# Kernel optimization log

Measured on AMD Instinct MI355X. Metric: run time of the kernel, lower is better.

## Reference

```python
import jax, jax.numpy as jnp
import numpy as np

N = 2_000_000
G = 10_000
NGQ = 5
_X_KS, _W_KS = np.polynomial.hermite.hermgauss(NGQ)


def setup_inputs() -> dict:
    key = jax.random.key(0)
    k1, k2, k3 = jax.random.split(key, 3)
    y_true = jax.random.bernoulli(k1, 0.5, (N, 1)).astype(jnp.float32)
    y_pred = jax.random.normal(k2, (N, 1), dtype=jnp.float32)
    Z_idx = jax.random.randint(k3, (N,), 0, G, dtype=jnp.int32)
    sig2b = jnp.array(1.0, dtype=jnp.float32)  # self.sig2bs[0]
    return {"y_true": y_true, "y_pred": y_pred, "sig2b": sig2b,
            "Z_idx": Z_idx, "n_groups": G}


def reference(y_true, y_pred, sig2b, Z_idx, n_groups):
    y = y_true[:, 0]  # [N]
    f = y_pred[:, 0]  # [N]
    x_ks = jnp.asarray(_X_KS, dtype=f.dtype)  # [K]
    w_ks = jnp.asarray(_W_KS, dtype=f.dtype)  # [K]
    # c_k = sqrt(2) * sqrt(sig2b) * x_k
    c = jnp.sqrt(jnp.asarray(2.0, f.dtype)) * jnp.sqrt(sig2b) * x_ks  # [K]
    # Per-group sufficient statistics (replaces the per-unique-group Python loop)
    yf_g = jax.ops.segment_sum(y * f, Z_idx, num_segments=n_groups)      # [G]
    ysum_g = jax.ops.segment_sum(y, Z_idx, num_segments=n_groups)        # [G]
    # log(1 + exp(f_i + c_k)) summed within each group -> [G, K]
    lg = jax.ops.segment_sum(jnp.log1p(jnp.exp(f[:, None] + c[None, :])),
                             Z_idx, num_segments=n_groups)
    expnt = yf_g[:, None] + ysum_g[:, None] * c[None, :] - lg            # [G, K]
    inv_sqrt_pi = 1.0 / np.sqrt(np.pi)
    k_sum = jnp.sum(jnp.exp(expnt) * (w_ks * inv_sqrt_pi)[None, :], axis=1)  # [G]
    total = -jnp.sum(jnp.log(k_sum))
    return total.reshape(1, 1)
```

## Files before the change

kernel.cpp:

```cpp
#include <hip/hip_runtime.h>
#include <math.h>


#define NG 10000
#define COPIES 256
#define ATHREADS 1024
#define ESCALE 16.0f
#define LN2ESC 11.090354888959125f
#define FMASK12 0xFFFull
#define LN2F 0.6931471805599453f
#define INVLN2F 1.4426950408889634f

__device__ __forceinline__ unsigned int spq(float x) {
    float e2 = __builtin_amdgcn_exp2f(-fabsf(x) * INVLN2F);
    float lg = __builtin_amdgcn_logf(1.0f + e2);
    return (unsigned int)(fmaxf(x, 0.0f) * ESCALE + lg * LN2ESC + 0.5f);
}

__device__ __forceinline__ unsigned long long compute_pack(float yi, float fi,
                                                           const float* ck) {
    float sy = 1.0f - 2.0f * yi;
    unsigned long long p = 0ull;
#pragma unroll
    for (int k = 0; k < 5; ++k) {
        unsigned int u = spq(sy * (fi + ck[k]));
        p |= (unsigned long long)u << (12 * k);
    }
    return p;
}


__global__ __launch_bounds__(ATHREADS) void copnll_accum_lds(
        const float* __restrict__ y, const float* __restrict__ f,
        const float* __restrict__ sig2b, const int* __restrict__ z,
        unsigned long long* __restrict__ partials,
        float* __restrict__ out, int n) {
    __shared__ __align__(16) unsigned long long lds[NG];

    const float s = sqrtf(2.0f) * sqrtf(sig2b[0]);
    const float xks[5] = {-2.0201828704560856f, -0.9585724646138185f, 0.0f,
                          0.9585724646138185f, 2.0201828704560856f};
    float ck[5];
#pragma unroll
    for (int k = 0; k < 5; ++k) ck[k] = s * xks[k];

    const float4* y4 = (const float4*)y;
    const float4* f4 = (const float4*)f;
    const int4*   z4 = (const int4*)z;
    int n4 = n >> 2;
    int t = blockIdx.x * ATHREADS + threadIdx.x;
    int total = gridDim.x * ATHREADS;
    int i0 = t, i1 = t + total;
    bool h0 = i0 < n4, h1 = i1 < n4;

    float4 ya, fa, yb, fb;
    int4 za, zb;
    if (h0) { ya = y4[i0]; fa = f4[i0]; za = z4[i0]; }
    if (h1) { yb = y4[i1]; fb = f4[i1]; zb = z4[i1]; }

    for (int j = threadIdx.x; j < NG; j += ATHREADS) lds[j] = 0ull;
    if (blockIdx.x == 0 && threadIdx.x == 0) out[0] = 0.0f;
    __syncthreads();

    if (h0) {
        atomicAdd(&lds[za.x], compute_pack(ya.x, fa.x, ck));
        atomicAdd(&lds[za.y], compute_pack(ya.y, fa.y, ck));
        atomicAdd(&lds[za.z], compute_pack(ya.z, fa.z, ck));
        atomicAdd(&lds[za.w], compute_pack(ya.w, fa.w, ck));
    }
    if (h1) {
        atomicAdd(&lds[zb.x], compute_pack(yb.x, fb.x, ck));
        atomicAdd(&lds[zb.y], compute_pack(yb.y, fb.y, ck));
        atomicAdd(&lds[zb.z], compute_pack(yb.z, fb.z, ck));
        atomicAdd(&lds[zb.w], compute_pack(yb.w, fb.w, ck));
    }
    for (int i = t + 2 * total; i < n4; i += total) {
        float4 yv = y4[i];
        float4 fv = f4[i];
        int4   zv = z4[i];
        atomicAdd(&lds[zv.x], compute_pack(yv.x, fv.x, ck));
        atomicAdd(&lds[zv.y], compute_pack(yv.y, fv.y, ck));
        atomicAdd(&lds[zv.z], compute_pack(yv.z, fv.z, ck));
        atomicAdd(&lds[zv.w], compute_pack(yv.w, fv.w, ck));
    }
    if (blockIdx.x == 0 && (int)threadIdx.x < (n & 3)) {
        int i = (n4 << 2) + threadIdx.x;
        atomicAdd(&lds[z[i]], compute_pack(y[i], f[i], ck));
    }
    __syncthreads();

    ulonglong2* dst = (ulonglong2*)(partials + (size_t)blockIdx.x * NG);
    const ulonglong2* src = (const ulonglong2*)lds;
    for (int j = threadIdx.x; j < NG / 2; j += ATHREADS) dst[j] = src[j];
}

#define GPB 64
#define SUBS 4
__global__ __launch_bounds__(256) void copnll_merge(
        const unsigned long long* __restrict__ partials,
        float* __restrict__ out) {
    const float wn[5] = {0.011257411327720683f, 0.22207592200561263f,
                         0.53333333333333333f, 0.22207592200561263f,
                         0.011257411327720683f};
    __shared__ unsigned int comb[SUBS][GPB][5];

    int gl  = threadIdx.x & 63;
    int sub = threadIdx.x >> 6;
    int g = blockIdx.x * GPB + gl;
    unsigned int fs0 = 0, fs1 = 0, fs2 = 0, fs3 = 0, fs4 = 0;
    if (g < NG) {
        const unsigned long long* base =
            partials + (size_t)sub * (COPIES / SUBS) * NG + g;
#pragma unroll 8
        for (int j = 0; j < COPIES / SUBS; ++j) {
            unsigned long long q = base[(size_t)j * NG];
            fs0 += (unsigned int)(q & FMASK12);
            fs1 += (unsigned int)((q >> 12) & FMASK12);
            fs2 += (unsigned int)((q >> 24) & FMASK12);
            fs3 += (unsigned int)((q >> 36) & FMASK12);
            fs4 += (unsigned int)((q >> 48) & FMASK12);
        }
    }
    comb[sub][gl][0] = fs0;
    comb[sub][gl][1] = fs1;
    comb[sub][gl][2] = fs2;
    comb[sub][gl][3] = fs3;
    comb[sub][gl][4] = fs4;
    __syncthreads();

    if (threadIdx.x < 64) {
        float local = 0.0f;
        if (g < NG) {
            unsigned int t0 = 0, t1 = 0, t2 = 0, t3 = 0, t4 = 0;
#pragma unroll
            for (int s2 = 0; s2 < SUBS; ++s2) {
                t0 += comb[s2][gl][0];
                t1 += comb[s2][gl][1];
                t2 += comb[s2][gl][2];
                t3 += comb[s2][gl][3];
                t4 += comb[s2][gl][4];
            }
            float ek[5];
            ek[0] = -(float)t0 * (1.0f / ESCALE);
            ek[1] = -(float)t1 * (1.0f / ESCALE);
            ek[2] = -(float)t2 * (1.0f / ESCALE);
            ek[3] = -(float)t3 * (1.0f / ESCALE);
            ek[4] = -(float)t4 * (1.0f / ESCALE);
            float m5 = ek[0];
#pragma unroll
            for (int k = 1; k < 5; ++k) m5 = fmaxf(m5, ek[k]);
            float ks = 0.0f;
#pragma unroll
            for (int k = 0; k < 5; ++k)
                ks += __builtin_amdgcn_exp2f((ek[k] - m5) * INVLN2F) * wn[k];
            local = m5 + LN2F * __builtin_amdgcn_logf(ks);
        }
#pragma unroll
        for (int off = 32; off > 0; off >>= 1)
            local += __shfl_down(local, off, 64);
        if (threadIdx.x == 0)
            atomicAdd(out, -local);
    }
}


#define EBIAS 18.0f
#define GSCALE 128.0f
#define FMASK21 0x1FFFFFull

__global__ __launch_bounds__(256) void copnll_zero_packs(
        unsigned long long* __restrict__ p, float* __restrict__ out) {
    int stride = gridDim.x * blockDim.x;
    for (int i = blockIdx.x * blockDim.x + threadIdx.x; i < 2 * NG; i += stride)
        p[i] = 0ull;
    if (blockIdx.x == 0 && threadIdx.x == 0) out[0] = 0.0f;
}

__global__ __launch_bounds__(256) void copnll_accum_atomic(
        const float* __restrict__ y, const float* __restrict__ f,
        const float* __restrict__ sig2b, const int* __restrict__ z,
        unsigned long long* __restrict__ packs, int n) {
    const float s = sqrtf(2.0f) * sqrtf(sig2b[0]);
    const float xks[5] = {-2.0201828704560856f, -0.9585724646138185f, 0.0f,
                          0.9585724646138185f, 2.0201828704560856f};
    int i = blockIdx.x * blockDim.x + threadIdx.x;
    if (i >= n) return;
    float sy = 1.0f - 2.0f * y[i], fi = f[i];
    unsigned int u[5];
#pragma unroll
    for (int k = 0; k < 5; ++k) {
        float x = sy * (fi + s * xks[k]);
        unsigned int uq = spq(x);
        u[k] = (unsigned int)(EBIAS * GSCALE + 0.5f) - uq * 8u;
    }
    unsigned long long p0 = (unsigned long long)u[0] |
                            ((unsigned long long)u[1] << 21) |
                            ((unsigned long long)u[2] << 42);
    unsigned long long p1 = (unsigned long long)u[3] |
                            ((unsigned long long)u[4] << 21) | (1ull << 42);
    int g = z[i];
    atomicAdd(&packs[g], p0);
    atomicAdd(&packs[NG + g], p1);
}

__global__ __launch_bounds__(256) void copnll_finalize_atomic(
        const unsigned long long* __restrict__ packs, float* __restrict__ out) {
    const float wn[5] = {0.011257411327720683f, 0.22207592200561263f,
                         0.53333333333333333f, 0.22207592200561263f,
                         0.011257411327720683f};
    int g = blockIdx.x * blockDim.x + threadIdx.x;
    float local = 0.0f;
    if (g < NG) {
        unsigned long long q0 = packs[g];
        unsigned long long q1 = packs[NG + g];
        float cnt = (float)(q1 >> 42);
        float off = EBIAS * cnt;
        float ek[5];
        ek[0] = (float)(q0 & FMASK21) * (1.0f / GSCALE) - off;
        ek[1] = (float)((q0 >> 21) & FMASK21) * (1.0f / GSCALE) - off;
        ek[2] = (float)((q0 >> 42) & FMASK21) * (1.0f / GSCALE) - off;
        ek[3] = (float)(q1 & FMASK21) * (1.0f / GSCALE) - off;
        ek[4] = (float)((q1 >> 21) & FMASK21) * (1.0f / GSCALE) - off;
        float m5 = ek[0];
#pragma unroll
        for (int k = 1; k < 5; ++k) m5 = fmaxf(m5, ek[k]);
        float ks = 0.0f;
#pragma unroll
        for (int k = 0; k < 5; ++k) ks += expf(ek[k] - m5) * wn[k];
        local = m5 + logf(ks);
    }
#pragma unroll
    for (int off = 32; off > 0; off >>= 1)
        local += __shfl_down(local, off, 64);
    if ((threadIdx.x & 63) == 0)
        atomicAdd(out, -local);
}

extern "C" void kernel_launch(void* const* d_in, const int* in_sizes, int n_in,
                              void* d_out, int out_size, void* d_ws, size_t ws_size,
                              hipStream_t stream) {
    const float* y_true = (const float*)d_in[0];
    const float* y_pred = (const float*)d_in[1];
    const float* sig2b  = (const float*)d_in[2];
    const int*   z_idx  = (const int*)d_in[3];
    int n = in_sizes[0];
    float* out = (float*)d_out;

    size_t need = (size_t)COPIES * NG * sizeof(unsigned long long);
    if (ws_size >= need) {
        unsigned long long* partials = (unsigned long long*)d_ws;
        copnll_accum_lds<<<COPIES, ATHREADS, 0, stream>>>(
            y_true, y_pred, sig2b, z_idx, partials, out, n);
        copnll_merge<<<(NG + GPB - 1) / GPB, 256, 0, stream>>>(partials, out);
    } else {
        unsigned long long* packs = (unsigned long long*)d_ws;
        copnll_zero_packs<<<64, 256, 0, stream>>>(packs, out);
        int blocks = (n + 255) / 256;
        copnll_accum_atomic<<<blocks, 256, 0, stream>>>(
            y_true, y_pred, sig2b, z_idx, packs, n);
        copnll_finalize_atomic<<<(NG + 255) / 256, 256, 0, stream>>>(packs, out);
    }
}
```

Before: 26.30 us.

## Use contiguous per-block chunks in accumulate and widen merge to 16 sub-reducers

The accumulate kernel now gives each block a contiguous range of float4 elements instead of a grid-stride loop. It also drops the early prefetch of the first two iterations, which had overlapped the global loads with LDS zeroing, and zeroes LDS first using 16-byte stores. The merge kernel moves from 256 to 1024 threads per block with 16 sub-reducers, so each thread reads 16 partial rows instead of 64. This shortens the merge's serial load chain and raises memory-level parallelism, at the cost of losing the load/zeroing overlap in the accumulate kernel.

```diff
diff --git a/kernel.cpp b/kernel.cpp
--- a/kernel.cpp
+++ b/kernel.cpp
@@ -37,6 +37,12 @@
         float* __restrict__ out, int n) {
     __shared__ __align__(16) unsigned long long lds[NG];
 
+    ulonglong2 zz; zz.x = 0ull; zz.y = 0ull;
+    ulonglong2* l2 = (ulonglong2*)lds;
+    for (int j = threadIdx.x; j < NG / 2; j += ATHREADS) l2[j] = zz;
+    if (blockIdx.x == 0 && threadIdx.x == 0) out[0] = 0.0f;
+    __syncthreads();
+
     const float s = sqrtf(2.0f) * sqrtf(sig2b[0]);
     const float xks[5] = {-2.0201828704560856f, -0.9585724646138185f, 0.0f,
                           0.9585724646138185f, 2.0201828704560856f};
@@ -48,33 +54,10 @@
     const float4* f4 = (const float4*)f;
     const int4*   z4 = (const int4*)z;
     int n4 = n >> 2;
-    int t = blockIdx.x * ATHREADS + threadIdx.x;
-    int total = gridDim.x * ATHREADS;
-    int i0 = t, i1 = t + total;
-    bool h0 = i0 < n4, h1 = i1 < n4;
-
-    float4 ya, fa, yb, fb;
-    int4 za, zb;
-    if (h0) { ya = y4[i0]; fa = f4[i0]; za = z4[i0]; }
-    if (h1) { yb = y4[i1]; fb = f4[i1]; zb = z4[i1]; }
-
-    for (int j = threadIdx.x; j < NG; j += ATHREADS) lds[j] = 0ull;
-    if (blockIdx.x == 0 && threadIdx.x == 0) out[0] = 0.0f;
-    __syncthreads();
-
-    if (h0) {
-        atomicAdd(&lds[za.x], compute_pack(ya.x, fa.x, ck));
-        atomicAdd(&lds[za.y], compute_pack(ya.y, fa.y, ck));
-        atomicAdd(&lds[za.z], compute_pack(ya.z, fa.z, ck));
-        atomicAdd(&lds[za.w], compute_pack(ya.w, fa.w, ck));
-    }
-    if (h1) {
-        atomicAdd(&lds[zb.x], compute_pack(yb.x, fb.x, ck));
-        atomicAdd(&lds[zb.y], compute_pack(yb.y, fb.y, ck));
-        atomicAdd(&lds[zb.z], compute_pack(yb.z, fb.z, ck));
-        atomicAdd(&lds[zb.w], compute_pack(yb.w, fb.w, ck));
-    }
-    for (int i = t + 2 * total; i < n4; i += total) {
+    int nb = (int)gridDim.x;
+    int beg = (int)(((long long)blockIdx.x * n4) / nb);
+    int end = (int)(((long long)(blockIdx.x + 1) * n4) / nb);
+    for (int i = beg + (int)threadIdx.x; i < end; i += ATHREADS) {
         float4 yv = y4[i];
         float4 fv = f4[i];
         int4   zv = z4[i];
@@ -95,14 +78,14 @@
 }
 
 #define GPB 64
-#define SUBS 4
-__global__ __launch_bounds__(256) void copnll_merge(
+#define MSUBS 16
+__global__ __launch_bounds__(1024) void copnll_merge(
         const unsigned long long* __restrict__ partials,
         float* __restrict__ out) {
     const float wn[5] = {0.011257411327720683f, 0.22207592200561263f,
                          0.53333333333333333f, 0.22207592200561263f,
                          0.011257411327720683f};
-    __shared__ unsigned int comb[SUBS][GPB][5];
+    __shared__ unsigned int comb[MSUBS][GPB][5];
 
     int gl  = threadIdx.x & 63;
     int sub = threadIdx.x >> 6;
@@ -110,9 +93,9 @@
     unsigned int fs0 = 0, fs1 = 0, fs2 = 0, fs3 = 0, fs4 = 0;
     if (g < NG) {
         const unsigned long long* base =
-            partials + (size_t)sub * (COPIES / SUBS) * NG + g;
-#pragma unroll 8
-        for (int j = 0; j < COPIES / SUBS; ++j) {
+            partials + (size_t)sub * (COPIES / MSUBS) * NG + g;
+#pragma unroll
+        for (int j = 0; j < COPIES / MSUBS; ++j) {
             unsigned long long q = base[(size_t)j * NG];
             fs0 += (unsigned int)(q & FMASK12);
             fs1 += (unsigned int)((q >> 12) & FMASK12);
@@ -133,7 +116,7 @@
         if (g < NG) {
             unsigned int t0 = 0, t1 = 0, t2 = 0, t3 = 0, t4 = 0;
 #pragma unroll
-            for (int s2 = 0; s2 < SUBS; ++s2) {
+            for (int s2 = 0; s2 < MSUBS; ++s2) {
                 t0 += comb[s2][gl][0];
                 t1 += comb[s2][gl][1];
                 t2 += comb[s2][gl][2];
@@ -251,7 +234,7 @@
         unsigned long long* partials = (unsigned long long*)d_ws;
         copnll_accum_lds<<<COPIES, ATHREADS, 0, stream>>>(
             y_true, y_pred, sig2b, z_idx, partials, out, n);
-        copnll_merge<<<(NG + GPB - 1) / GPB, 256, 0, stream>>>(partials, out);
+        copnll_merge<<<(NG + GPB - 1) / GPB, 1024, 0, stream>>>(partials, out);
     } else {
         unsigned long long* packs = (unsigned long long*)d_ws;
         copnll_zero_packs<<<64, 256, 0, stream>>>(packs, out);
```

Result: faster. 23.41 us (-11.0%).
